# Optimization experiments

Hardware: AMD Instinct MI355X
Metric: run time of the kernel (lower is better)

## Reference

```python
import jax, jax.numpy as jnp
import numpy as np
from jax import lax

D_VOCAB = 262
D_EMB = 128
CONV_W = 5
PAD = CONV_W // 2  # 2


def setup_inputs() -> dict:
    key = jax.random.key(0)
    k1, k2, k3, k4, k5 = jax.random.split(key, 5)
    B, W, C = 128, 256, 16
    input = jax.random.randint(k1, (B, W, C), 0, D_VOCAB, dtype=jnp.int64)
    lengths = jax.random.randint(k2, (B, W), 1, C + 1, dtype=jnp.int64)
    # torch init: Embedding weight ~ N(0,1) then *0.1
    emb_weight = jax.random.normal(k3, (D_VOCAB, D_EMB), dtype=jnp.float32) * 0.1
    fan_in = D_EMB * CONV_W
    bound = 1.0 / np.sqrt(fan_in)
    conv_w = jax.random.uniform(k4, (D_EMB, D_EMB, CONV_W), dtype=jnp.float32, minval=-bound, maxval=bound)
    conv_b = jax.random.uniform(k5, (D_EMB,), dtype=jnp.float32, minval=-bound, maxval=bound)
    return {"input": input, "lengths": lengths, "emb_weight": emb_weight,
            "conv_w": conv_w, "conv_b": conv_b}


def reference(input, lengths, emb_weight, conv_w, conv_b):
    B, W, C = input.shape
    ids = input.reshape(B * W, C)                      # [N, C]
    embed = emb_weight[ids]                            # [N, C, E] gather
    x = jnp.transpose(embed, (0, 2, 1))                # [N, E, C] (NCW)
    y = lax.conv_general_dilated(
        x, conv_w,
        window_strides=(1,), padding=[(PAD, PAD)],
        dimension_numbers=("NCH", "OIH", "NCH"))       # [N, E, C]
    y = y + conv_b[None, :, None]
    out = jnp.max(y, axis=-1)                          # max-pool over chars
    return out.reshape(B, W, -1)                       # [B, W, E]
```

## Files before the change

kernel.cpp:

```cpp
#include <hip/hip_runtime.h>
#include <hip/hip_fp16.h>

#define D_VOCAB 262
#define D_EMB   128
#define KW      5
#define NCHAR   16
#define NKO     (KW * D_EMB)

typedef _Float16 h2 __attribute__((ext_vector_type(2)));
typedef _Float16 h8 __attribute__((ext_vector_type(8)));


__global__ __launch_bounds__(256) void transpose_w_kernel(
    const float* __restrict__ cw, float* __restrict__ Wt2) {
  const int gid = blockIdx.x * 256 + threadIdx.x;
  const float val = cw[gid];
  const int o = gid / 640;
  const int r = gid - o * 640;
  const int i = r / 5;
  const int k = r - i * 5;
  Wt2[i * NKO + k * D_EMB + o] = val;
}

__global__ __launch_bounds__(128) void compute_P_kernel(
    const float* __restrict__ emb, const float* __restrict__ Wt2,
    __half* __restrict__ P) {
  __shared__ float emb_s[D_EMB];
  const int b = blockIdx.x;
  const int v = b / KW;
  const int k = b - v * KW;
  const int t = threadIdx.x;
  emb_s[t] = emb[v * D_EMB + t];
  __syncthreads();

  const float* col = Wt2 + k * D_EMB + t;
  float acc = 0.f;
#pragma unroll 16
  for (int i = 0; i < D_EMB; ++i) {
    acc += emb_s[i] * col[i * NKO];
  }
  P[v * NKO + k * D_EMB + t] = __float2half(acc);
}

__global__ __launch_bounds__(256) void conv_char_main_kernel(
    const int* __restrict__ ids, const _Float16* __restrict__ P,
    const float* __restrict__ bias, float* __restrict__ out) {
  const int lane = threadIdx.x & 63;
  int n = (int)((blockIdx.x * 256 + threadIdx.x) >> 6);
  n = __builtin_amdgcn_readfirstlane(n);

  const int* idrow = ids + n * NCHAR;
  const int o = lane * 2;

  h2 win[5];
#pragma unroll
  for (int w = 0; w < 5; ++w) win[w] = (h2)(_Float16)0.f;
  h2 vmax = (h2)(_Float16)(-60000.f);

#pragma unroll
  for (int j = 0; j < NCHAR; ++j) {
    const int id = idrow[j];
    const _Float16* row = P + (size_t)id * NKO + o;
#pragma unroll
    for (int k = 0; k < KW; ++k) {
      const int c = j + 2 - k;
      if (c >= 0 && c < NCHAR) {
        const h2 val = *(const h2*)(row + k * D_EMB);
        win[c % 5] += val;
      }
    }
    if (j >= 2) {
      const int w = (j - 2) % 5;
      vmax = __builtin_elementwise_max(vmax, win[w]);
      win[w] = (h2)(_Float16)0.f;
    }
  }
  vmax = __builtin_elementwise_max(vmax, win[14 % 5]);
  vmax = __builtin_elementwise_max(vmax, win[15 % 5]);

  const float2 bv = *(const float2*)(bias + o);
  float2 r;
  r.x = (float)vmax.x + bv.x;
  r.y = (float)vmax.y + bv.y;
  *(float2*)(out + (size_t)n * D_EMB + o) = r;
}

extern "C" void kernel_launch(void* const* d_in, const int* in_sizes, int n_in,
                              void* d_out, int out_size, void* d_ws, size_t ws_size,
                              hipStream_t stream) {
  const int*   input = (const int*)d_in[0];
  const float* emb   = (const float*)d_in[2];
  const float* cw    = (const float*)d_in[3];
  const float* cb    = (const float*)d_in[4];
  float* out = (float*)d_out;

  _Float16* P   = (_Float16*)d_ws;
  float*    Wt2 = (float*)((char*)d_ws + 335872);

  const int n_seq = in_sizes[0] / NCHAR;

  transpose_w_kernel<<<320, 256, 0, stream>>>(cw, Wt2);
  compute_P_kernel<<<D_VOCAB * KW, 128, 0, stream>>>(emb, Wt2, (__half*)P);

  const int blocks = n_seq / 4;
  conv_char_main_kernel<<<blocks, 256, 0, stream>>>(input, P, cb, out);
}
```

Before: 94.08 us.

## Process four sequences per wave with 16-byte loads and shuffled ids

Each wave now handles four sequences instead of one: 16 lanes per sequence, each lane owning 8 output channels and loading h8 (16-byte) rows from the projected table. Character ids are loaded once per lane and distributed with lane shuffles rather than read as scalar loads per character. The goal is wider memory transactions, fewer instructions per output, and less per-wave overhead. The cost is a quarter as many waves and more registers per lane, so there is less latency hiding.

```diff
diff --git a/kernel.cpp b/kernel.cpp
--- a/kernel.cpp
+++ b/kernel.cpp
@@ -46,43 +46,56 @@
     const int* __restrict__ ids, const _Float16* __restrict__ P,
     const float* __restrict__ bias, float* __restrict__ out) {
   const int lane = threadIdx.x & 63;
-  int n = (int)((blockIdx.x * 256 + threadIdx.x) >> 6);
-  n = __builtin_amdgcn_readfirstlane(n);
+  const int wave = (int)((blockIdx.x * 256 + threadIdx.x) >> 6);
+  const int seq0 = wave << 2;
+  const int t    = lane & 15;
+  const int grp  = lane >> 4;
 
-  const int* idrow = ids + n * NCHAR;
-  const int o = lane * 2;
+  const int myid = ids[seq0 * NCHAR + lane];
 
-  h2 win[5];
+  h8 win[5];
 #pragma unroll
-  for (int w = 0; w < 5; ++w) win[w] = (h2)(_Float16)0.f;
-  h2 vmax = (h2)(_Float16)(-60000.f);
+  for (int w = 0; w < 5; ++w) win[w] = (h8)(_Float16)0.f;
+  h8 vmax = (h8)(_Float16)(-60000.f);
+
+  const _Float16* Pl = P + t * 8;
 
 #pragma unroll
   for (int j = 0; j < NCHAR; ++j) {
-    const int id = idrow[j];
-    const _Float16* row = P + (size_t)id * NKO + o;
+    const int idj = __shfl(myid, (lane & 48) | j);
+    const _Float16* row = Pl + idj * NKO;
 #pragma unroll
     for (int k = 0; k < KW; ++k) {
       const int c = j + 2 - k;
       if (c >= 0 && c < NCHAR) {
-        const h2 val = *(const h2*)(row + k * D_EMB);
+        const h8 val = *(const h8*)(row + k * D_EMB);
         win[c % 5] += val;
       }
     }
     if (j >= 2) {
       const int w = (j - 2) % 5;
       vmax = __builtin_elementwise_max(vmax, win[w]);
-      win[w] = (h2)(_Float16)0.f;
+      win[w] = (h8)(_Float16)0.f;
     }
   }
   vmax = __builtin_elementwise_max(vmax, win[14 % 5]);
   vmax = __builtin_elementwise_max(vmax, win[15 % 5]);
 
-  const float2 bv = *(const float2*)(bias + o);
-  float2 r;
-  r.x = (float)vmax.x + bv.x;
-  r.y = (float)vmax.y + bv.y;
-  *(float2*)(out + (size_t)n * D_EMB + o) = r;
+  const int o = t * 8;
+  const float4 b0 = *(const float4*)(bias + o);
+  const float4 b1 = *(const float4*)(bias + o + 4);
+  float* op = out + (size_t)(seq0 + grp) * D_EMB + o;
+  float4 r0, r1;
+  r0.x = (float)vmax[0] + b0.x;
+  r0.y = (float)vmax[1] + b0.y;
+  r0.z = (float)vmax[2] + b0.z;
+  r0.w = (float)vmax[3] + b0.w;
+  r1.x = (float)vmax[4] + b1.x;
+  r1.y = (float)vmax[5] + b1.y;
+  r1.z = (float)vmax[6] + b1.z;
+  r1.w = (float)vmax[7] + b1.w;
+  *(float4*)op = r0;
+  *(float4*)(op + 4) = r1;
 }
 
 extern "C" void kernel_launch(void* const* d_in, const int* in_sizes, int n_in,
@@ -102,6 +115,6 @@
   transpose_w_kernel<<<320, 256, 0, stream>>>(cw, Wt2);
   compute_P_kernel<<<D_VOCAB * KW, 128, 0, stream>>>(emb, Wt2, (__half*)P);
 
-  const int blocks = n_seq / 4;
+  const int blocks = n_seq / 16;
   conv_char_main_kernel<<<blocks, 256, 0, stream>>>(input, P, cb, out);
 }
```

Result: no change. 94.36 us (+0.3%).
